# Performance work log

Measured on AMD Instinct MI355X. Metric: run time of the kernel, lower is better.

## Reference

```python
import jax, jax.numpy as jnp
import numpy as np

N = 50000          # nodes
E = 1_600_000      # edges (avg degree 32)
F_IN = 128         # num_node_features
HID = 128          # hidden_dim
G = 512            # graphs in batch
NEG_SLOPE = 0.2    # PyG GATConv default


def setup_inputs() -> dict:
    key = jax.random.key(0)
    ks = jax.random.split(key, 13)
    s_in = 1.0 / np.sqrt(F_IN)
    s_h = 1.0 / np.sqrt(HID)
    return {
        "x": jax.random.normal(ks[0], (N, F_IN), jnp.float32),
        "edge_index": jax.random.randint(ks[1], (2, E), 0, N, dtype=jnp.int32),
        "batch": jnp.sort(jax.random.randint(ks[2], (N,), 0, G, dtype=jnp.int32)),
        "W1": jax.random.normal(ks[3], (F_IN, HID), jnp.float32) * s_in,
        "a_src1": jax.random.normal(ks[4], (HID,), jnp.float32) * s_h,
        "a_dst1": jax.random.normal(ks[5], (HID,), jnp.float32) * s_h,
        "b1": jnp.zeros((HID,), jnp.float32),
        "W2": jax.random.normal(ks[6], (HID, HID), jnp.float32) * s_h,
        "a_src2": jax.random.normal(ks[7], (HID,), jnp.float32) * s_h,
        "a_dst2": jax.random.normal(ks[8], (HID,), jnp.float32) * s_h,
        "b2": jnp.zeros((HID,), jnp.float32),
        "fc_w": jax.random.normal(ks[9], (2 * HID, 1), jnp.float32) * (1.0 / np.sqrt(2 * HID)),
        "fc_b": jnp.zeros((1,), jnp.float32),
    }


def _gat_conv(x, W, a_src, a_dst, b, src, dst, n):
    # PyG GATConv, heads=1: h = xW; alpha_e = softmax_dst(leaky_relu(a_s.h[src] + a_d.h[dst]))
    h = x @ W                                    # [N, C]
    asrc = h @ a_src                             # [N]
    adst = h @ a_dst                             # [N]
    logits = jax.nn.leaky_relu(asrc[src] + adst[dst], NEG_SLOPE)  # [E']
    m = jax.ops.segment_max(logits, dst, num_segments=n)
    ex = jnp.exp(logits - m[dst])
    denom = jax.ops.segment_sum(ex, dst, num_segments=n)
    alpha = ex / denom[dst]                      # segment softmax over incoming edges
    out = jax.ops.segment_sum(h[src] * alpha[:, None], dst, num_segments=n)
    return out + b


def reference(x, edge_index, batch, W1, a_src1, a_dst1, b1, W2, a_src2, a_dst2, b2, fc_w, fc_b):
    n = x.shape[0]
    loop = jnp.arange(n, dtype=edge_index.dtype)   # add_self_loops=True (PyG default)
    src = jnp.concatenate([edge_index[0], loop])
    dst = jnp.concatenate([edge_index[1], loop])

    h = jax.nn.relu(x)
    h = jax.nn.relu(_gat_conv(h, W1, a_src1, a_dst1, b1, src, dst, n))
    h = jax.nn.relu(_gat_conv(h, W2, a_src2, a_dst2, b2, src, dst, n))

    counts = jax.ops.segment_sum(jnp.ones((n,), h.dtype), batch, num_segments=G)
    maxp = jax.ops.segment_max(h, batch, num_segments=G)
    maxp = jnp.where(counts[:, None] > 0, maxp, 0.0)
    meanp = jax.ops.segment_sum(h, batch, num_segments=G) / jnp.maximum(counts, 1.0)[:, None]
    pooled = jnp.concatenate([maxp, meanp], axis=1)  # [G, 2*HID]
    return pooled @ fc_w + fc_b                      # [G, 1]
```

## Files before the change

### kernel.cpp

```cpp
#include <hip/hip_runtime.h>
#include <math.h>


#define LEAKY 0.2f
#define CAP 128

__device__ __forceinline__ unsigned short f2bf(float x) {
    unsigned int u = __float_as_uint(x);
    unsigned int r = (u + 0x7FFFu + ((u >> 16) & 1u)) >> 16;
    return (unsigned short)r;
}
__device__ __forceinline__ float bf2f(unsigned short b) {
    return __uint_as_float((unsigned int)b << 16);
}

__global__ __launch_bounds__(256) void scatterx(const int* __restrict__ ei,
                                                int* __restrict__ cnt,
                                                unsigned short* __restrict__ col,
                                                int E, int N) {
    const int g = blockIdx.x & 7;
    const int chunk = blockIdx.x >> 3;
    const int lo = (int)(((long long)N * g) >> 3);
    const int hi = (int)(((long long)N * (g + 1)) >> 3);
    const int base = chunk * 4096;
    int fin = base + 4096; if (fin > E) fin = E;
    for (int i = base + threadIdx.x; i < fin; i += 256) {
        int d = ei[E + i];
        if (d >= lo && d < hi) {
            int s = ei[i];
            int pos = atomicAdd(&cnt[d], 1);
            if (pos < CAP) col[(size_t)d * CAP + pos] = (unsigned short)s;
        }
    }
}

__global__ __launch_bounds__(256) void gemm64(const float* __restrict__ A,
                                              const float* __restrict__ B,
                                              float* __restrict__ C,
                                              unsigned short* __restrict__ Cb,
                                              const float* __restrict__ a_src,
                                              const float* __restrict__ a_dst,
                                              float* __restrict__ asv,
                                              float* __restrict__ adv,
                                              int n, int applyRelu) {
    __shared__ float Ast[32][68];
    __shared__ float Bs[32][132];
    __shared__ float sredS[64][17];
    __shared__ float sredD[64][17];
    const int tid = threadIdx.x;
    const int row0 = blockIdx.x * 64;
    const int tx = tid & 15;
    const int ty = tid >> 4;
    float acc[4][8] = {};

    for (int k0 = 0; k0 < 128; k0 += 32) {
        {
            int kv = tid & 7, r = tid >> 3;
            int kk = kv * 4;
#pragma unroll
            for (int i = 0; i < 2; ++i) {
                int rr = r + 32 * i;
                int grow = row0 + rr;
                float4 v = make_float4(0.f, 0.f, 0.f, 0.f);
                if (grow < n) {
                    v = *(const float4*)(A + (size_t)grow * 128 + k0 + kk);
                    if (applyRelu) {
                        v.x = fmaxf(v.x, 0.f); v.y = fmaxf(v.y, 0.f);
                        v.z = fmaxf(v.z, 0.f); v.w = fmaxf(v.w, 0.f);
                    }
                }
                Ast[kk + 0][rr] = v.x;
                Ast[kk + 1][rr] = v.y;
                Ast[kk + 2][rr] = v.z;
                Ast[kk + 3][rr] = v.w;
            }
        }
        {
            int cv = tid & 31, kr = tid >> 5;
#pragma unroll
            for (int i = 0; i < 4; ++i) {
                int kk2 = kr + 8 * i;
                float4 v = *(const float4*)(B + (size_t)(k0 + kk2) * 128 + cv * 4);
                Bs[kk2][cv * 4 + 0] = v.x; Bs[kk2][cv * 4 + 1] = v.y;
                Bs[kk2][cv * 4 + 2] = v.z; Bs[kk2][cv * 4 + 3] = v.w;
            }
        }
        __syncthreads();
#pragma unroll
        for (int k = 0; k < 32; ++k) {
            float4 a4 = *(const float4*)&Ast[k][ty * 4];
            float4 q0 = *(const float4*)&Bs[k][tx * 8];
            float4 q1 = *(const float4*)&Bs[k][tx * 8 + 4];
            float a[4] = { a4.x, a4.y, a4.z, a4.w };
            float b[8] = { q0.x, q0.y, q0.z, q0.w, q1.x, q1.y, q1.z, q1.w };
#pragma unroll
            for (int i = 0; i < 4; ++i)
#pragma unroll
                for (int j = 0; j < 8; ++j) acc[i][j] += a[i] * b[j];
        }
        __syncthreads();
    }

    float asl[8], adl[8];
#pragma unroll
    for (int j = 0; j < 8; ++j) {
        asl[j] = a_src[tx * 8 + j];
        adl[j] = a_dst[tx * 8 + j];
    }
#pragma unroll
    for (int i = 0; i < 4; ++i) {
        int rr = ty * 4 + i;
        int grow = row0 + rr;
        float ps = 0.f, pd = 0.f;
#pragma unroll
        for (int j = 0; j < 8; ++j) {
            ps += acc[i][j] * asl[j];
            pd += acc[i][j] * adl[j];
        }
        sredS[rr][tx] = ps;
        sredD[rr][tx] = pd;
        if (grow < n) {
            float4* dst = (float4*)(C + (size_t)grow * 128 + tx * 8);
            dst[0] = make_float4(acc[i][0], acc[i][1], acc[i][2], acc[i][3]);
            dst[1] = make_float4(acc[i][4], acc[i][5], acc[i][6], acc[i][7]);
            uint4 pk;
            pk.x = (unsigned)f2bf(acc[i][0]) | ((unsigned)f2bf(acc[i][1]) << 16);
            pk.y = (unsigned)f2bf(acc[i][2]) | ((unsigned)f2bf(acc[i][3]) << 16);
            pk.z = (unsigned)f2bf(acc[i][4]) | ((unsigned)f2bf(acc[i][5]) << 16);
            pk.w = (unsigned)f2bf(acc[i][6]) | ((unsigned)f2bf(acc[i][7]) << 16);
            *(uint4*)(Cb + (size_t)grow * 128 + tx * 8) = pk;
        }
    }
    __syncthreads();
    if (tid < 64) {
        int grow = row0 + tid;
        if (grow < n) {
            float ps = 0.f, pd = 0.f;
#pragma unroll
            for (int j = 0; j < 16; ++j) {
                ps += sredS[tid][j];
                pd += sredD[tid][j];
            }
            asv[grow] = ps;
            adv[grow] = pd;
        }
    }
}

__global__ __launch_bounds__(256) void aggregate(const unsigned short* __restrict__ hb,
                                                 const int* __restrict__ cnt,
                                                 const unsigned short* __restrict__ col,
                                                 const float* __restrict__ asv,
                                                 const float* __restrict__ adv,
                                                 const float* __restrict__ bias,
                                                 float* __restrict__ out, int n) {
    __shared__ int   scol[4][128];
    __shared__ float swt[4][128];
    const int wv = threadIdx.x >> 6;
    const int lane = threadIdx.x & 63;
    const int w = blockIdx.x * 4 + wv;
    if (w >= n) return;
    int deg = cnt[w];
    if (deg > CAP - 1) deg = CAP - 1;
    const int D = deg + 1;
    const size_t start = (size_t)w * CAP;
    const float ad = adv[w];

    int c0 = 0, c1 = 0;
    float l0 = -INFINITY, l1 = -INFINITY;
    if (lane < D) {
        c0 = (lane < deg) ? (int)col[start + lane] : w;
        l0 = asv[c0] + ad;
        l0 = l0 > 0.f ? l0 : LEAKY * l0;
    }
    if (64 + lane < D) {
        c1 = (64 + lane < deg) ? (int)col[start + 64 + lane] : w;
        l1 = asv[c1] + ad;
        l1 = l1 > 0.f ? l1 : LEAKY * l1;
    }
    float m = fmaxf(l0, l1);
#pragma unroll
    for (int off = 32; off; off >>= 1) m = fmaxf(m, __shfl_xor(m, off, 64));
    float e0 = (lane < D) ? __expf(l0 - m) : 0.f;
    float e1 = (64 + lane < D) ? __expf(l1 - m) : 0.f;
    float s = e0 + e1;
#pragma unroll
    for (int off = 32; off; off >>= 1) s += __shfl_xor(s, off, 64);
    float inv = 1.f / s;
    if (lane < D)      { scol[wv][lane] = c0;      swt[wv][lane] = e0; }
    if (64 + lane < D) { scol[wv][64 + lane] = c1; swt[wv][64 + lane] = e1; }

    const int hw = lane >> 5;
    const int sl = lane & 31;
    float4 aa[8];
#pragma unroll
    for (int j = 0; j < 8; ++j) aa[j] = make_float4(0.f, 0.f, 0.f, 0.f);
    for (int i = 0; i < D; i += 16) {
        int cs[8]; float ws[8];
#pragma unroll
        for (int j = 0; j < 8; ++j) {
            int idx = i + 2 * j + hw;
            int cl = idx < D ? idx : D - 1;
            cs[j] = scol[wv][cl];
            ws[j] = (idx < D) ? swt[wv][idx] : 0.f;
        }
        ushort4 rs[8];
#pragma unroll
        for (int j = 0; j < 8; ++j)
            rs[j] = *((const ushort4*)(hb + (size_t)cs[j] * 128) + sl);
#pragma unroll
        for (int j = 0; j < 8; ++j) {
            aa[j].x += ws[j] * bf2f(rs[j].x);
            aa[j].y += ws[j] * bf2f(rs[j].y);
            aa[j].z += ws[j] * bf2f(rs[j].z);
            aa[j].w += ws[j] * bf2f(rs[j].w);
        }
    }
#pragma unroll
    for (int j = 1; j < 8; ++j) {
        aa[0].x += aa[j].x; aa[0].y += aa[j].y;
        aa[0].z += aa[j].z; aa[0].w += aa[j].w;
    }
    aa[0].x += __shfl_xor(aa[0].x, 32);
    aa[0].y += __shfl_xor(aa[0].y, 32);
    aa[0].z += __shfl_xor(aa[0].z, 32);
    aa[0].w += __shfl_xor(aa[0].w, 32);
    if (hw == 0) {
        float4 b = ((const float4*)bias)[sl];
        float4 o;
        o.x = fmaxf(aa[0].x * inv + b.x, 0.f);
        o.y = fmaxf(aa[0].y * inv + b.y, 0.f);
        o.z = fmaxf(aa[0].z * inv + b.z, 0.f);
        o.w = fmaxf(aa[0].w * inv + b.w, 0.f);
        *((float4*)(out + (size_t)w * 128) + sl) = o;
    }
}

__global__ __launch_bounds__(128) void poolfc(const float* __restrict__ h2,
                                              const int* __restrict__ batch,
                                              const float* __restrict__ fcw,
                                              const float* __restrict__ fcb,
                                              float* __restrict__ out, int G, int n) {
    __shared__ int seg[2];
    int g = blockIdx.x;
    int f = threadIdx.x;
    if (f < 2) {
        int target = g + f;
        int lo = 0, hi = n;
        while (lo < hi) {
            int mid = (lo + hi) >> 1;
            if (batch[mid] < target) lo = mid + 1; else hi = mid;
        }
        seg[f] = lo;
    }
    __syncthreads();
    int s = seg[0], e = seg[1];
    float m = -INFINITY, sum = 0.f;
    for (int node = s; node < e; ++node) {
        float v = h2[(size_t)node * 128 + f];
        m = fmaxf(m, v);
        sum += v;
    }
    int cnt = e - s;
    float maxp = (cnt > 0) ? m : 0.f;
    float cden = (float)(cnt > 0 ? cnt : 1);
    float meanp = sum / cden;
    float p = maxp * fcw[f] + meanp * fcw[128 + f];
    __shared__ float red[128];
    red[f] = p;
    __syncthreads();
    for (int off = 64; off; off >>= 1) {
        if (f < off) red[f] += red[f + off];
        __syncthreads();
    }
    if (f == 0) out[g] = red[0] + fcb[0];
}

extern "C" void kernel_launch(void* const* d_in, const int* in_sizes, int n_in,
                              void* d_out, int out_size, void* d_ws, size_t ws_size,
                              hipStream_t stream) {
    const int N = in_sizes[0] / 128;
    const int E = in_sizes[1] / 2;
    const int G = out_size;

    const float* x      = (const float*)d_in[0];
    const int*   ei     = (const int*)d_in[1];
    const int*   batch  = (const int*)d_in[2];
    const float* W1     = (const float*)d_in[3];
    const float* a_src1 = (const float*)d_in[4];
    const float* a_dst1 = (const float*)d_in[5];
    const float* b1     = (const float*)d_in[6];
    const float* W2     = (const float*)d_in[7];
    const float* a_src2 = (const float*)d_in[8];
    const float* a_dst2 = (const float*)d_in[9];
    const float* b2     = (const float*)d_in[10];
    const float* fcw    = (const float*)d_in[11];
    const float* fcb    = (const float*)d_in[12];
    float* out = (float*)d_out;

    char* wp = (char*)d_ws;
    auto alloc = [&](size_t bytes) -> void* {
        void* p = (void*)wp;
        wp += (bytes + 255) & ~(size_t)255;
        return p;
    };
    int* cnt     = (int*)alloc(sizeof(int) * N);
    unsigned short* col = (unsigned short*)alloc(sizeof(unsigned short) * (size_t)N * CAP);
    float* hp    = (float*)alloc(sizeof(float) * (size_t)N * 128);
    float* ha    = (float*)alloc(sizeof(float) * (size_t)N * 128);
    unsigned short* hb = (unsigned short*)alloc(sizeof(unsigned short) * (size_t)N * 128);
    float* asv   = (float*)alloc(sizeof(float) * N);
    float* adv   = (float*)alloc(sizeof(float) * N);

    hipMemsetAsync(cnt, 0, sizeof(int) * N, stream);

    const int gemmGrid = (N + 63) / 64;
    const int waveGrid = (N + 3) / 4;
    const int nchunk = (E + 4095) / 4096;

    scatterx<<<nchunk * 8, 256, 0, stream>>>(ei, cnt, col, E, N);

    gemm64<<<gemmGrid, 256, 0, stream>>>(x, W1, hp, hb, a_src1, a_dst1, asv, adv, N, 1);
    aggregate<<<waveGrid, 256, 0, stream>>>(hb, cnt, col, asv, adv, b1, ha, N);

    gemm64<<<gemmGrid, 256, 0, stream>>>(ha, W2, hp, hb, a_src2, a_dst2, asv, adv, N, 0);
    aggregate<<<waveGrid, 256, 0, stream>>>(hb, cnt, col, asv, adv, b2, ha, N);

    poolfc<<<G, 128, 0, stream>>>(ha, batch, fcw, fcb, out, G, N);
}
```

Baseline: 391.2 us.

## Fuse edge scatter into first GEMM launch and vectorize edge index loads

Merges the CSR-building scatter kernel into the first layer GEMM kernel by appending scatter blocks after the GEMM blocks in one grid. This removes a separate launch and lets the atomic scatter work overlap with the GEMM on idle compute units. Edge indices are now read as int4 vectors, four edges per thread per step. The trade-offs are a larger shared-memory footprint for the scatter blocks and possible contention between them.

Measured after the change: 374.9 us. 4.2% less time.

```diff
diff --git a/kernel.cpp b/kernel.cpp
--- a/kernel.cpp
+++ b/kernel.cpp
@@ -14,39 +14,59 @@
     return __uint_as_float((unsigned int)b << 16);
 }
 
-__global__ __launch_bounds__(256) void scatterx(const int* __restrict__ ei,
+__global__ __launch_bounds__(256) void gemmscat(const float* __restrict__ A,
+                                                const float* __restrict__ B,
+                                                float* __restrict__ C,
+                                                unsigned short* __restrict__ Cb,
+                                                const float* __restrict__ a_src,
+                                                const float* __restrict__ a_dst,
+                                                float* __restrict__ asv,
+                                                float* __restrict__ adv,
+                                                int n, int applyRelu,
+                                                int gemmBlocks,
+                                                const int* __restrict__ ei,
                                                 int* __restrict__ cnt,
                                                 unsigned short* __restrict__ col,
-                                                int E, int N) {
-    const int g = blockIdx.x & 7;
-    const int chunk = blockIdx.x >> 3;
-    const int lo = (int)(((long long)N * g) >> 3);
-    const int hi = (int)(((long long)N * (g + 1)) >> 3);
-    const int base = chunk * 4096;
-    int fin = base + 4096; if (fin > E) fin = E;
-    for (int i = base + threadIdx.x; i < fin; i += 256) {
-        int d = ei[E + i];
-        if (d >= lo && d < hi) {
-            int s = ei[i];
-            int pos = atomicAdd(&cnt[d], 1);
-            if (pos < CAP) col[(size_t)d * CAP + pos] = (unsigned short)s;
-        }
-    }
-}
-
-__global__ __launch_bounds__(256) void gemm64(const float* __restrict__ A,
-                                              const float* __restrict__ B,
-                                              float* __restrict__ C,
-                                              unsigned short* __restrict__ Cb,
-                                              const float* __restrict__ a_src,
-                                              const float* __restrict__ a_dst,
-                                              float* __restrict__ asv,
-                                              float* __restrict__ adv,
-                                              int n, int applyRelu) {
+                                                int E) {
     __shared__ float Ast[32][68];
     __shared__ float Bs[32][132];
     __shared__ float sredS[64][17];
     __shared__ float sredD[64][17];
+
+    if ((int)blockIdx.x >= gemmBlocks) {
+        const int b = (int)blockIdx.x - gemmBlocks;
+        const int g = (int)blockIdx.x & 7;
+        const int lo = (int)(((long long)n * g) >> 3);
+        const int hi = (int)(((long long)n * (g + 1)) >> 3);
+        const int base = (b >> 3) * 4096;
+        int4 dv[4], sv[4];
+        int ok[4];
+#pragma unroll
+        for (int t = 0; t < 4; ++t) {
+            int i0 = base + t * 1024 + (int)threadIdx.x * 4;
+            ok[t] = (i0 < E);
+            if (ok[t]) {
+                dv[t] = *(const int4*)(ei + (size_t)E + i0);
+                sv[t] = *(const int4*)(ei + i0);
+            }
+        }
+#pragma unroll
+        for (int t = 0; t < 4; ++t) {
+            if (!ok[t]) continue;
+            int dd[4] = { dv[t].x, dv[t].y, dv[t].z, dv[t].w };
+            int ss[4] = { sv[t].x, sv[t].y, sv[t].z, sv[t].w };
+#pragma unroll
+            for (int j = 0; j < 4; ++j) {
+                int d = dd[j];
+                if (d >= lo && d < hi) {
+                    int pos = atomicAdd(&cnt[d], 1);
+                    if (pos < CAP) col[(size_t)d * CAP + pos] = (unsigned short)ss[j];
+                }
+            }
+        }
+        return;
+    }
+
     const int tid = threadIdx.x;
     const int row0 = blockIdx.x * 64;
     const int tx = tid & 15;
@@ -316,14 +336,14 @@
 
     const int gemmGrid = (N + 63) / 64;
     const int waveGrid = (N + 3) / 4;
-    const int nchunk = (E + 4095) / 4096;
-
-    scatterx<<<nchunk * 8, 256, 0, stream>>>(ei, cnt, col, E, N);
-
-    gemm64<<<gemmGrid, 256, 0, stream>>>(x, W1, hp, hb, a_src1, a_dst1, asv, adv, N, 1);
+    const int scatGrid = ((E + 4095) / 4096) * 8;
+
+    gemmscat<<<gemmGrid + scatGrid, 256, 0, stream>>>(
+        x, W1, hp, hb, a_src1, a_dst1, asv, adv, N, 1, gemmGrid, ei, cnt, col, E);
     aggregate<<<waveGrid, 256, 0, stream>>>(hb, cnt, col, asv, adv, b1, ha, N);
 
-    gemm64<<<gemmGrid, 256, 0, stream>>>(ha, W2, hp, hb, a_src2, a_dst2, asv, adv, N, 0);
+    gemmscat<<<gemmGrid, 256, 0, stream>>>(
+        ha, W2, hp, hb, a_src2, a_dst2, asv, adv, N, 0, gemmGrid, ei, cnt, col, E);
     aggregate<<<waveGrid, 256, 0, stream>>>(hb, cnt, col, asv, adv, b2, ha, N);
 
     poolfc<<<G, 128, 0, stream>>>(ha, batch, fcw, fcb, out, G, N);
```
